# Kernel tuning notes

Hardware: AMD Instinct MI355X
Metric: run time of the kernel (lower is better)

The kernel has to match this reference:

```python
import jax, jax.numpy as jnp
import numpy as np

NUM_EMBEDDINGS = 1024
EMBEDDING_DIM = 256
COMMITMENT_COST = 0.02


def setup_inputs() -> dict:
    key = jax.random.key(0)
    k1, k2 = jax.random.split(key)
    z = jax.random.normal(k1, (64, 256, 32, 32), dtype=jnp.float32)
    # torch init: uniform(-1/K, 1/K)
    emb = jax.random.uniform(k2, (NUM_EMBEDDINGS, EMBEDDING_DIM), dtype=jnp.float32,
                             minval=-1.0 / NUM_EMBEDDINGS, maxval=1.0 / NUM_EMBEDDINGS)
    return {"z": z, "emb": emb}


def reference(z, emb):
    n, d, h, w = z.shape
    # (N, D, H, W) -> (N*H*W, D)
    z_flat = jnp.transpose(z, (0, 2, 3, 1)).reshape(-1, d)
    # squared L2 distances: ||z||^2 - 2 z.E^T + ||E||^2  -> (NHW, K)
    distances = (jnp.sum(z_flat * z_flat, axis=1, keepdims=True)
                 - 2.0 * z_flat @ emb.T
                 + jnp.sum(emb * emb, axis=1))
    indices = jnp.argmin(distances, axis=1)  # (NHW,)
    z_q = jnp.transpose(emb[indices].reshape(n, h, w, d), (0, 3, 1, 2))  # (N, D, H, W)
    # straight-through estimator
    z_q_st = z + jax.lax.stop_gradient(z_q - z)
    commitment_loss = COMMITMENT_COST * jnp.mean((jax.lax.stop_gradient(z) - z_q) ** 2)
    codebook_loss = jnp.mean((z - jax.lax.stop_gradient(z_q)) ** 2)
    vq_loss = commitment_loss + codebook_loss
    indices_reshaped = indices.reshape(n, h, w)
    return z_q_st, indices_reshaped, vq_loss
```

## Files before the change

kernel.cpp:

```cpp
#include <hip/hip_runtime.h>
#include <hip/hip_bf16.h>
#include <float.h>

#define OUT_IDX_OFF 16777216
#define OUT_LOSS_OFF 16842752
#define CAND_OFF 8388608
#define GMIN_OFF 12582912
#define GCNT_OFF 13107200
#define NSLOT 32
#define DELTA 2.0e-3f

typedef __attribute__((ext_vector_type(8))) short short8;
typedef __attribute__((ext_vector_type(4))) float f32x4;

static __device__ __forceinline__ unsigned short f2bf(float f) {
  union { __hip_bfloat16 h; unsigned short u; } cv;
  cv.h = __float2bfloat16(f);
  return cv.u;
}

__global__ __launch_bounds__(256) void k_prep(const float* __restrict__ emb,
                                              unsigned short* __restrict__ E2,
                                              float* __restrict__ cws,
                                              int* __restrict__ gmin,
                                              int* __restrict__ gcnt,
                                              float* __restrict__ out) {
  const int k = blockIdx.x, d = threadIdx.x;
  const int tid = (k << 8) + d;
  if (tid < 65536) {
    gmin[tid] = 0x7f7f7f7f;
    gcnt[tid] = 0;
  }
  if (tid == 0) out[OUT_LOSS_OFF] = 0.0f;
  const float v = emb[k * 256 + d];
  __shared__ float red[256];
  __shared__ unsigned short row[256];
  row[d] = f2bf(v);
  red[d] = v * v;
  __syncthreads();
  for (int s = 128; s > 0; s >>= 1) {
    if (d < s) red[d] += red[d + s];
    __syncthreads();
  }
  if (d == 0) cws[k] = red[0];
  if (d < 32) ((short8*)&E2[k * 256])[d] = ((short8*)row)[d];
}

__global__ __launch_bounds__(256) void k_cvt4(const float* __restrict__ z,
                                              unsigned short* __restrict__ A2,
                                              float* __restrict__ aws) {
#pragma clang fp contract(off)
  __shared__ float tile[64][65];
  __shared__ float red2[128];
  const int t = threadIdx.x;
  const int p0 = blockIdx.x << 6;
  const int n = p0 >> 10, hw0 = p0 & 1023;
  const float* zb = z + (size_t)n * 262144 + hw0;
  const int hwl = (t & 15) << 2;
  const int dlb = t >> 4;
  const int row = t & 63, h = (t >> 6) & 1;
  const int pl = t >> 2, c = t & 3;

  float4 v[4];
#pragma unroll
  for (int i = 0; i < 4; ++i)
    v[i] = *(const float4*)&zb[(size_t)(dlb + i * 16) * 1024 + hwl];

  float acc[8];

  for (int dt = 0; dt < 4; ++dt) {
    if (dt) __syncthreads();
#pragma unroll
    for (int i = 0; i < 4; ++i) {
      const int dl = dlb + i * 16;
      tile[hwl + 0][dl] = v[i].x;
      tile[hwl + 1][dl] = v[i].y;
      tile[hwl + 2][dl] = v[i].z;
      tile[hwl + 3][dl] = v[i].w;
    }
    __syncthreads();
    if (dt < 3) {
      const float* zb2 = zb + (size_t)(dt + 1) * 65536;
#pragma unroll
      for (int i = 0; i < 4; ++i)
        v[i] = *(const float4*)&zb2[(size_t)(dlb + i * 16) * 1024 + hwl];
    }
    unsigned short* dst = &A2[(size_t)(p0 + pl) * 256 + dt * 64];
#pragma unroll
    for (int hh = 0; hh < 2; ++hh) {
      const int ch = c + hh * 4;
      unsigned short tmp[8];
#pragma unroll
      for (int j = 0; j < 8; ++j) tmp[j] = f2bf(tile[pl][ch * 8 + j]);
      *(short8*)&dst[ch * 8] = *(short8*)tmp;
    }
    if (t < 128 && (dt >> 1) == h) {
      if ((dt & 1) == 0) {
#pragma unroll
        for (int j = 0; j < 8; ++j) {
          const float x = tile[row][j];
          acc[j] = x * x;
        }
        for (int g = 1; g < 8; ++g)
#pragma unroll
          for (int j = 0; j < 8; ++j) {
            const float x = tile[row][g * 8 + j];
            const float p = x * x;
            acc[j] = acc[j] + p;
          }
      } else {
        for (int g = 8; g < 16; ++g)
#pragma unroll
          for (int j = 0; j < 8; ++j) {
            const float x = tile[row][(g - 8) * 8 + j];
            const float p = x * x;
            acc[j] = acc[j] + p;
          }
      }
    }
  }
  if (t < 128) {
    const float s = ((acc[0] + acc[1]) + (acc[2] + acc[3])) +
                    ((acc[4] + acc[5]) + (acc[6] + acc[7]));
    red2[t] = s;
  }
  __syncthreads();
  if (t < 64) aws[p0 + t] = red2[t] + red2[t + 64];
}

__global__ __launch_bounds__(256, 4) void k_gemm9(
    const unsigned short* __restrict__ A2, const unsigned short* __restrict__ E2,
    const float* __restrict__ cws, const float* __restrict__ aws,
    int* __restrict__ gmin, int* __restrict__ gcnt,
    float2* __restrict__ gcand) {
  __shared__ __align__(16) unsigned short As[128 * 64];
  __shared__ __align__(16) unsigned short Bs[128 * 64];
  __shared__ float a_l[128], c_l[128], rmkt[256], bmin[128];

  const int t = threadIdx.x;
  const int lane = t & 63;
  const int wave = __builtin_amdgcn_readfirstlane(t >> 6);
  const int wr = wave >> 1, wc = wave & 1;
  const int quad = lane >> 4, l15 = lane & 15;
  const int swa = l15 & 7;

  const int bid = blockIdx.x;
  const int L = ((bid & 7) << 9) + (bid >> 3);
  const int rb = L >> 3, ck = L & 7;
  const int r0 = rb << 7, k0 = ck << 7;

  if (t < 128) {
    a_l[t] = aws[r0 + t];
    c_l[t] = cws[k0 + t];
  }

  const int srow = t >> 3;
  const int gpos = t & 7;

  f32x4 acc[4][4];
#pragma unroll
  for (int a = 0; a < 4; ++a)
#pragma unroll
    for (int b = 0; b < 4; ++b) acc[a][b] = (f32x4)(0.0f);

  for (int kt = 0; kt < 4; ++kt) {
    if (kt) __syncthreads();
#pragma unroll
    for (int i = 0; i < 4; ++i) {
      const int row = (i << 5) + srow;
      const int gsrc = gpos ^ (row & 7);
      const unsigned short* sa =
          A2 + (((size_t)(r0 + row)) << 8) + (kt << 6) + (gsrc << 3);
      __builtin_amdgcn_global_load_lds(
          (const __attribute__((address_space(1))) void*)sa,
          (__attribute__((address_space(3))) void*)(As + (i << 11) +
                                                    (wave << 9)),
          16, 0, 0);
      const unsigned short* sb =
          E2 + (((size_t)(k0 + row)) << 8) + (kt << 6) + (gsrc << 3);
      __builtin_amdgcn_global_load_lds(
          (const __attribute__((address_space(1))) void*)sb,
          (__attribute__((address_space(3))) void*)(Bs + (i << 11) +
                                                    (wave << 9)),
          16, 0, 0);
    }
    __syncthreads();
#pragma unroll
    for (int ks = 0; ks < 2; ++ks) {
      short8 af[4], bf[4];
#pragma unroll
      for (int tr = 0; tr < 4; ++tr)
        af[tr] = *(const short8*)&As[(wr * 64 + tr * 16 + l15) * 64 +
                                     (((ks * 4 + quad) ^ swa) << 3)];
#pragma unroll
      for (int tc = 0; tc < 4; ++tc)
        bf[tc] = *(const short8*)&Bs[(wc * 64 + tc * 16 + l15) * 64 +
                                     (((ks * 4 + quad) ^ swa) << 3)];
#pragma unroll
      for (int tr = 0; tr < 4; ++tr)
#pragma unroll
        for (int tc = 0; tc < 4; ++tc)
          acc[tr][tc] = __builtin_amdgcn_mfma_f32_16x16x32_bf16(
              af[tr], bf[tc], acc[tr][tc], 0, 0, 0);
    }
  }

#pragma unroll
  for (int tr = 0; tr < 4; ++tr)
#pragma unroll
    for (int rg = 0; rg < 4; ++rg) {
      const int rloc = wr * 64 + tr * 16 + quad * 4 + rg;
      const float av = a_l[rloc];
      float mn = FLT_MAX;
#pragma unroll
      for (int tc = 0; tc < 4; ++tc) {
        const int cloc = wc * 64 + tc * 16 + l15;
        const float s = av + fmaf(-2.0f, acc[tr][tc][rg], c_l[cloc]);
        mn = fminf(mn, s);
      }
      mn = fminf(mn, __shfl_xor(mn, 1));
      mn = fminf(mn, __shfl_xor(mn, 2));
      mn = fminf(mn, __shfl_xor(mn, 4));
      mn = fminf(mn, __shfl_xor(mn, 8));
      if (l15 == 0) rmkt[rloc * 2 + wc] = mn;
    }
  __syncthreads();
  if (t < 128) {
    const float m = fminf(rmkt[t * 2], rmkt[t * 2 + 1]);
    const int old = atomicMin(&gmin[r0 + t], __float_as_int(m));
    bmin[t] = fminf(m, __int_as_float(old));
  }
  __syncthreads();
#pragma unroll
  for (int tr = 0; tr < 4; ++tr)
#pragma unroll
    for (int rg = 0; rg < 4; ++rg) {
      const int rloc = wr * 64 + tr * 16 + quad * 4 + rg;
      const float av = a_l[rloc];
      const float lim = bmin[rloc] + DELTA;
#pragma unroll
      for (int tc = 0; tc < 4; ++tc) {
        const int cloc = wc * 64 + tc * 16 + l15;
        const float s = av + fmaf(-2.0f, acc[tr][tc][rg], c_l[cloc]);
        if (s <= lim) {
          const int pos = atomicAdd(&gcnt[r0 + rloc], 1);
          if (pos < NSLOT)
            gcand[(size_t)(r0 + rloc) * NSLOT + pos] =
                make_float2(s, __int_as_float(k0 + cloc));
        }
      }
    }
}

__global__ __launch_bounds__(256) void k_finish(
    const float* __restrict__ z, const float* __restrict__ emb,
    const float* __restrict__ cws, const float* __restrict__ aws,
    const int* __restrict__ gmin, const int* __restrict__ gcnt,
    const float2* __restrict__ gcand, int* __restrict__ idxws,
    float* __restrict__ out) {
  const int tid = (blockIdx.x << 8) + threadIdx.x;
  const int r = tid >> 2, sub = tid & 3;
  const float lim = __int_as_float(gmin[r]) + DELTA;
  int m = gcnt[r];
  if (m > NSLOT) m = NSLOT;
  const int n = r >> 10, hw = r & 1023;
  const float* zp = z + (size_t)n * 262144 + hw;
  const float a = aws[r];
  float bestv = FLT_MAX;
  int besti = 0x7fffffff;
  for (int ci = sub; ci < m; ci += 4) {
    const float2 p = gcand[(size_t)r * NSLOT + ci];
    if (p.x > lim) continue;
    const int k = __float_as_int(p.y);
    const float* ep = emb + (size_t)k * 256;
    float dot = 0.0f;
#pragma unroll 8
    for (int d = 0; d < 256; ++d) dot = fmaf(zp[(size_t)d * 1024], ep[d], dot);
    float s = fmaf(-2.0f, dot, a);
    s = s + cws[k];
    if (s < bestv || (s == bestv && k < besti)) {
      bestv = s;
      besti = k;
    }
  }
#pragma unroll
  for (int off = 1; off < 4; off <<= 1) {
    const float ov = __shfl_xor(bestv, off);
    const int oi = __shfl_xor(besti, off);
    if (ov < bestv || (ov == bestv && oi < besti)) {
      bestv = ov;
      besti = oi;
    }
  }
  if (sub == 0) {
    idxws[r] = besti;
    out[OUT_IDX_OFF + r] = (float)besti;
  }
  float c = (sub == 0) ? bestv : 0.0f;
#pragma unroll
  for (int off = 1; off < 64; off <<= 1) c += __shfl_xor(c, off);
  if ((threadIdx.x & 63) == 0)
    atomicAdd(&out[OUT_LOSS_OFF], c * (1.02f / 16777216.0f));
}

__global__ __launch_bounds__(256) void k_out2(const float* __restrict__ emb,
                                              const int* __restrict__ idxws,
                                              float* __restrict__ out) {
  __shared__ float zq[32][257];
  __shared__ int sidx[32];
  const int t = threadIdx.x;
  const int p0 = blockIdx.x << 5;
  const int n = p0 >> 10, hw0 = p0 & 1023;
  if (t < 32) sidx[t] = idxws[p0 + t];
  __syncthreads();
#pragma unroll
  for (int it = 0; it < 8; ++it) {
    const int i = t + (it << 8);
    const int p = i >> 6;
    const int q = (i & 63) << 2;
    const float4 v = *(const float4*)&emb[(size_t)sidx[p] * 256 + q];
    zq[p][q] = v.x;
    zq[p][q + 1] = v.y;
    zq[p][q + 2] = v.z;
    zq[p][q + 3] = v.w;
  }
  __syncthreads();
  const int p = t & 31, d0 = t >> 5;
  float* ob = out + (size_t)n * 262144 + hw0 + p;
#pragma unroll
  for (int dd = 0; dd < 32; ++dd) {
    const int d = (dd << 3) + d0;
    ob[(size_t)d * 1024] = zq[p][d];
  }
}

extern "C" void kernel_launch(void* const* d_in, const int* in_sizes, int n_in,
                              void* d_out, int out_size, void* d_ws,
                              size_t ws_size, hipStream_t stream) {
  const float* z = (const float*)d_in[0];
  const float* emb = (const float*)d_in[1];
  float* out = (float*)d_out;

  unsigned short* E2 = (unsigned short*)d_ws;
  float* cws = (float*)(E2 + 262144);
  float* aws = cws + 1024;
  int* idxws = (int*)(aws + 65536);
  unsigned short* A2 = (unsigned short*)d_out;
  float2* gcand = (float2*)(out + CAND_OFF);
  int* gmin = (int*)(out + GMIN_OFF);
  int* gcnt = (int*)(out + GCNT_OFF);

  k_prep<<<dim3(1024), dim3(256), 0, stream>>>(emb, E2, cws, gmin, gcnt, out);
  k_cvt4<<<dim3(1024), dim3(256), 0, stream>>>(z, A2, aws);
  k_gemm9<<<dim3(4096), dim3(256), 0, stream>>>(A2, E2, cws, aws, gmin, gcnt,
                                                gcand);
  k_finish<<<dim3(1024), dim3(256), 0, stream>>>(z, emb, cws, aws, gmin, gcnt,
                                                 gcand, idxws, out);
  k_out2<<<dim3(2048), dim3(256), 0, stream>>>(emb, idxws, out);
}
```

Before: 295.9 us.

## Fuse codebook gather into finish kernel using workspace for candidate buffers

When the workspace is large enough, the candidate lists, min and count buffers move from the output tensor into workspace, so the finish kernel can write z_q directly into the output and the separate gather/transpose kernel is skipped. The finish kernel now uses one thread per row instead of four threads per row with shuffle reduction. This drops a launch and the idx round trip, at the cost of less parallelism in the candidate rescoring (256 blocks instead of 1024) and uncoalesced-per-thread but row-contiguous stores of z_q.

```diff
diff --git a/kernel.cpp b/kernel.cpp
--- a/kernel.cpp
+++ b/kernel.cpp
@@ -252,14 +252,13 @@
     }
 }
 
-__global__ __launch_bounds__(256) void k_finish(
+__global__ __launch_bounds__(256) void k_finish2(
     const float* __restrict__ z, const float* __restrict__ emb,
     const float* __restrict__ cws, const float* __restrict__ aws,
     const int* __restrict__ gmin, const int* __restrict__ gcnt,
     const float2* __restrict__ gcand, int* __restrict__ idxws,
-    float* __restrict__ out) {
-  const int tid = (blockIdx.x << 8) + threadIdx.x;
-  const int r = tid >> 2, sub = tid & 3;
+    float* __restrict__ out, int write_zq) {
+  const int r = (blockIdx.x << 8) + threadIdx.x;
   const float lim = __int_as_float(gmin[r]) + DELTA;
   int m = gcnt[r];
   if (m > NSLOT) m = NSLOT;
@@ -268,7 +267,7 @@
   const float a = aws[r];
   float bestv = FLT_MAX;
   int besti = 0x7fffffff;
-  for (int ci = sub; ci < m; ci += 4) {
+  for (int ci = 0; ci < m; ++ci) {
     const float2 p = gcand[(size_t)r * NSLOT + ci];
     if (p.x > lim) continue;
     const int k = __float_as_int(p.y);
@@ -283,20 +282,22 @@
       besti = k;
     }
   }
-#pragma unroll
-  for (int off = 1; off < 4; off <<= 1) {
-    const float ov = __shfl_xor(bestv, off);
-    const int oi = __shfl_xor(besti, off);
-    if (ov < bestv || (ov == bestv && oi < besti)) {
-      bestv = ov;
-      besti = oi;
-    }
-  }
-  if (sub == 0) {
+  out[OUT_IDX_OFF + r] = (float)besti;
+  if (write_zq) {
+    float* ob = out + (size_t)n * 262144 + hw;
+    const float4* e4 = (const float4*)(emb + (size_t)besti * 256);
+#pragma unroll 4
+    for (int d0 = 0; d0 < 64; ++d0) {
+      const float4 e = e4[d0];
+      ob[(size_t)(d0 * 4 + 0) * 1024] = e.x;
+      ob[(size_t)(d0 * 4 + 1) * 1024] = e.y;
+      ob[(size_t)(d0 * 4 + 2) * 1024] = e.z;
+      ob[(size_t)(d0 * 4 + 3) * 1024] = e.w;
+    }
+  } else {
     idxws[r] = besti;
-    out[OUT_IDX_OFF + r] = (float)besti;
-  }
-  float c = (sub == 0) ? bestv : 0.0f;
+  }
+  float c = bestv;
 #pragma unroll
   for (int off = 1; off < 64; off <<= 1) c += __shfl_xor(c, off);
   if ((threadIdx.x & 63) == 0)
@@ -346,15 +347,28 @@
   float* aws = cws + 1024;
   int* idxws = (int*)(aws + 65536);
   unsigned short* A2 = (unsigned short*)d_out;
-  float2* gcand = (float2*)(out + CAND_OFF);
-  int* gmin = (int*)(out + GMIN_OFF);
-  int* gcnt = (int*)(out + GCNT_OFF);
+
+  const size_t WS_NEED = 1052672u + 262144u + 262144u + 16777216u;
+  const int big_ws = (ws_size >= WS_NEED) ? 1 : 0;
+  int* gmin;
+  int* gcnt;
+  float2* gcand;
+  if (big_ws) {
+    gmin = idxws + 65536;
+    gcnt = gmin + 65536;
+    gcand = (float2*)(gcnt + 65536);
+  } else {
+    gcand = (float2*)(out + CAND_OFF);
+    gmin = (int*)(out + GMIN_OFF);
+    gcnt = (int*)(out + GCNT_OFF);
+  }
 
   k_prep<<<dim3(1024), dim3(256), 0, stream>>>(emb, E2, cws, gmin, gcnt, out);
   k_cvt4<<<dim3(1024), dim3(256), 0, stream>>>(z, A2, aws);
   k_gemm9<<<dim3(4096), dim3(256), 0, stream>>>(A2, E2, cws, aws, gmin, gcnt,
                                                 gcand);
-  k_finish<<<dim3(1024), dim3(256), 0, stream>>>(z, emb, cws, aws, gmin, gcnt,
-                                                 gcand, idxws, out);
-  k_out2<<<dim3(2048), dim3(256), 0, stream>>>(emb, idxws, out);
-}
+  k_finish2<<<dim3(256), dim3(256), 0, stream>>>(z, emb, cws, aws, gmin, gcnt,
+                                                 gcand, idxws, out, big_ws);
+  if (!big_ws)
+    k_out2<<<dim3(2048), dim3(256), 0, stream>>>(emb, idxws, out);
+}
```

After: 347.0 us. +17.3%, slower.
